# Kernel tuning notes

Measured on AMD Instinct MI355X. Metric: run time of the kernel, lower is better.

## Reference

```python
import jax, jax.numpy as jnp
import numpy as np

MAX_DISP = 48
PATCH = 3
OFFSET = 0
PAD = PATCH // 2
EPS = 1e-3


def _unfold(x, P, pad):
    # x: [B,C,H,W] -> [B,C,K2,H,W], K2 enumerated row-major over the PxP window
    B, C, H, W = x.shape
    xp = jnp.pad(x, ((0, 0), (0, 0), (pad, pad), (pad, pad)))
    return jnp.stack([xp[:, :, i:i + H, j:j + W]
                      for i in range(P) for j in range(P)], axis=2)


def _normalize(x, axes):
    # torch F.normalize: x / clamp(||x||_2, min=eps)
    n = jnp.sqrt(jnp.sum(x * x, axis=axes, keepdims=True))
    return x / jnp.maximum(n, EPS)


def setup_inputs() -> dict:
    key = jax.random.key(0)
    k1, k2, k3 = jax.random.split(key, 3)
    shp = (2, 32, 128, 416)
    return {
        "xl": jax.random.normal(k1, shp, dtype=jnp.float32),
        "xm": jax.random.normal(k2, shp, dtype=jnp.float32),
        "xr": jax.random.normal(k3, shp, dtype=jnp.float32),
    }


def reference(xl, xm, xr):
    B, C, H, W = xl.shape
    K2 = PATCH * PATCH
    scale = (C * K2) ** 0.5

    pl = _normalize(_unfold(xl, PATCH, PAD), (1, 2))  # [B,C,K2,H,W]
    pr = _normalize(_unfold(xr, PATCH, PAD), (1, 2))
    fl = _normalize(xm, (1,))                          # [B,C,H,W]

    # fl is constant over the K2 axis, so sum patches over K2 once for sim_L/sim_R
    Sl = pl.sum(axis=2)  # [B,C,H,W]
    Sr = pr.sum(axis=2)

    cL, cR, cLR = [], [], []
    for d in range(OFFSET, OFFSET + MAX_DISP):
        if d > 0:
            # shifted_l[w] = patches_l[w+d] (zero right pad); shifted_r[w] = patches_r[w-d]
            sL = jnp.einsum('bchw,bchw->bhw', fl[..., :W - d], Sl[..., d:])
            sL = jnp.pad(sL, ((0, 0), (0, 0), (0, d)))
            sR = jnp.einsum('bchw,bchw->bhw', fl[..., d:], Sr[..., :W - d])
            sR = jnp.pad(sR, ((0, 0), (0, 0), (d, 0)))
            wlr = W - 2 * d  # overlap region of the two opposite shifts
            if wlr > 0:
                sLR = jnp.einsum('bckhw,bckhw->bhw', pl[..., 2 * d:], pr[..., :wlr])
                sLR = jnp.pad(sLR, ((0, 0), (0, 0), (d, d)))
            else:
                sLR = jnp.zeros((B, H, W), xl.dtype)
        else:
            sL = jnp.einsum('bchw,bchw->bhw', fl, Sl)
            sR = jnp.einsum('bchw,bchw->bhw', fl, Sr)
            sLR = jnp.einsum('bckhw,bckhw->bhw', pl, pr)
        cL.append(sL / scale)
        cR.append(sR / scale)
        cLR.append(sLR / scale)

    cost = jnp.stack([jnp.stack(cL, 1), jnp.stack(cR, 1), jnp.stack(cLR, 1)], axis=1)
    return jnp.clip(cost, -10.0, 10.0).astype(jnp.float16)  # [B,3,D,H,W]
```

## Files before the change

### kernel.cpp

```cpp
#include <hip/hip_runtime.h>
#include <math.h>

#define B 2
#define C 32
#define H 128
#define W 416
#define D 48
#define HW (H*W)
#define CHW (C*HW)
#define EPSN 1e-3f
#define ISCALE 0.05892556509887896f
#define LSTR 36
#define DSPL (D / 2)

__device__ __forceinline__ float clip10(float x) {
    return fminf(fmaxf(x, -10.0f), 10.0f);
}

__global__ __launch_bounds__(256) void k_sq(const float* __restrict__ xl,
                                            const float* __restrict__ xr,
                                            const float* __restrict__ xm,
                                            float* __restrict__ sql,
                                            float* __restrict__ sqr,
                                            float* __restrict__ inm) {
    int idx = blockIdx.x * 256 + threadIdx.x;
    if (idx >= B * HW) return;
    int b = idx / HW, hw = idx - b * HW;
    const float* pl = xl + (size_t)b * CHW + hw;
    const float* pr = xr + (size_t)b * CHW + hw;
    const float* pm = xm + (size_t)b * CHW + hw;
    float al = 0.f, ar = 0.f, am = 0.f;
#pragma unroll
    for (int c = 0; c < C; ++c) {
        float vl = pl[c * HW], vr = pr[c * HW], vm = pm[c * HW];
        al += vl * vl; ar += vr * vr; am += vm * vm;
    }
    sql[idx] = al;
    sqr[idx] = ar;
    inm[idx] = 1.0f / fmaxf(sqrtf(am), EPSN);
}

__global__ __launch_bounds__(256) void k_norm(const float* __restrict__ sql,
                                              const float* __restrict__ sqr,
                                              float* __restrict__ inl,
                                              float* __restrict__ inr) {
    int idx = blockIdx.x * 256 + threadIdx.x;
    if (idx >= B * HW) return;
    int b = idx / HW, hw = idx - b * HW;
    int h = hw / W, w = hw - h * W;
    float sl = 0.f, sr = 0.f;
#pragma unroll
    for (int di = -1; di <= 1; ++di) {
        int hh = h + di;
        if (hh < 0 || hh >= H) continue;
#pragma unroll
        for (int dj = -1; dj <= 1; ++dj) {
            int ww = w + dj;
            if (ww < 0 || ww >= W) continue;
            int p = b * HW + hh * W + ww;
            sl += sql[p];
            sr += sqr[p];
        }
    }
    inl[idx] = 1.0f / fmaxf(sqrtf(sl), EPSN);
    inr[idx] = 1.0f / fmaxf(sqrtf(sr), EPSN);
}

__global__ __launch_bounds__(256) void k_box(const float* __restrict__ xl,
                                             const float* __restrict__ xr,
                                             float* __restrict__ boxl,
                                             float* __restrict__ boxr) {
    int idx = blockIdx.x * 256 + threadIdx.x;
    int w4 = (idx % (W / 4)) * 4;
    int h = (idx / (W / 4)) % H;
    int rest = idx / (H * (W / 4));
    size_t base = (size_t)rest * HW;
    float4 al = {0.f, 0.f, 0.f, 0.f}, ar = {0.f, 0.f, 0.f, 0.f};
#pragma unroll
    for (int dh = -1; dh <= 1; ++dh) {
        int hh = h + dh;
        if (hh < 0 || hh >= H) continue;
        const float* rl = xl + base + hh * W;
        const float* rr = xr + base + hh * W;
        float4 m = *(const float4*)(rl + w4);
        float lm = (w4 > 0) ? rl[w4 - 1] : 0.f;
        float rm = (w4 + 4 < W) ? rl[w4 + 4] : 0.f;
        al.x += lm + m.x + m.y;  al.y += m.x + m.y + m.z;
        al.z += m.y + m.z + m.w; al.w += m.z + m.w + rm;
        float4 n = *(const float4*)(rr + w4);
        float ln = (w4 > 0) ? rr[w4 - 1] : 0.f;
        float rn = (w4 + 4 < W) ? rr[w4 + 4] : 0.f;
        ar.x += ln + n.x + n.y;  ar.y += n.x + n.y + n.z;
        ar.z += n.y + n.z + n.w; ar.w += n.z + n.w + rn;
    }
    *(float4*)(boxl + base + h * W + w4) = al;
    *(float4*)(boxr + base + h * W + w4) = ar;
}

__device__ __forceinline__ void stage_row_v2(const float* __restrict__ gsrc,
                                             float* __restrict__ lds,
                                             int tid, int nthreads) {
    for (int t = tid; t < (W / 4) * C; t += nthreads) {
        int rw = t & 7;
        int cl = (t >> 3) & 7;
        int g  = t >> 6;
        int wg = g % 13;
        int ch = g / 13;
        int c  = ch * 8 + cl;
        int w4 = (wg * 8 + rw) * 4;
        float4 v = *(const float4*)(gsrc + (size_t)c * HW + w4);
        lds[(w4 + 0) * LSTR + c] = v.x;
        lds[(w4 + 1) * LSTR + c] = v.y;
        lds[(w4 + 2) * LSTR + c] = v.z;
        lds[(w4 + 3) * LSTR + c] = v.w;
    }
}

__device__ __forceinline__ float dot32(const float* __restrict__ fl,
                                       const float* __restrict__ col) {
    const float4* c4 = (const float4*)col;
    float a = 0.0f;
#pragma unroll
    for (int q = 0; q < 8; ++q) {
        float4 v = c4[q];
        a += fl[4 * q + 0] * v.x + fl[4 * q + 1] * v.y
           + fl[4 * q + 2] * v.z + fl[4 * q + 3] * v.w;
    }
    return a;
}

__device__ __forceinline__ void dot32x2(const float* __restrict__ fl0,
                                        const float* __restrict__ fl1,
                                        const float* __restrict__ col,
                                        float& a0, float& a1) {
    const float4* c4 = (const float4*)col;
    float s0 = 0.f, s1 = 0.f;
#pragma unroll
    for (int q = 0; q < 8; ++q) {
        float4 v = c4[q];
        s0 += fl0[4 * q + 0] * v.x + fl0[4 * q + 1] * v.y
            + fl0[4 * q + 2] * v.z + fl0[4 * q + 3] * v.w;
        s1 += fl1[4 * q + 0] * v.x + fl1[4 * q + 1] * v.y
            + fl1[4 * q + 2] * v.z + fl1[4 * q + 3] * v.w;
    }
    a0 = s0; a1 = s1;
}

__global__ __launch_bounds__(256) void k_lr(const float* __restrict__ xm,
                                            const float* __restrict__ boxl,
                                            const float* __restrict__ boxr,
                                            const float* __restrict__ inl,
                                            const float* __restrict__ inr,
                                            const float* __restrict__ inm,
                                            float* __restrict__ out) {
    __shared__ float sB[W * LSTR];
    __shared__ float sIn[W];
    int tid = threadIdx.x;
    int h = blockIdx.x;
    int b = blockIdx.y;
    int d0 = blockIdx.z * DSPL;
    bool act = tid < (W / 2);
    int w = 2 * tid;
    int bhw = b * HW + h * W;
    const float* pm = xm + (size_t)b * CHW + h * W;

    float fl0[C], fl1[C];
    if (act) {
        float2 im = *(const float2*)(inm + bhw + w);
#pragma unroll
        for (int c = 0; c < C; ++c) {
            float2 mv = *(const float2*)(pm + c * HW + w);
            fl0[c] = mv.x * im.x;
            fl1[c] = mv.y * im.y;
        }
    } else {
#pragma unroll
        for (int c = 0; c < C; ++c) { fl0[c] = 0.f; fl1[c] = 0.f; }
    }

    stage_row_v2(boxl + (size_t)b * CHW + h * W, sB, tid, 256);
    for (int j = tid; j < W; j += 256) sIn[j] = inl[bhw + j];
    __syncthreads();
    if (act) {
        float* o = out + ((size_t)b * 3 + 0) * D * HW + h * W;
        float a0p = 0.f;
#pragma unroll 4
        for (int j = 0; j <= DSPL; ++j) {
            int v = w + d0 + j;
            float a0 = 0.f, a1 = 0.f;
            if (v < W) {
                dot32x2(fl0, fl1, sB + v * LSTR, a0, a1);
                float s = sIn[v] * ISCALE;
                a0 = clip10(a0 * s);
                a1 = clip10(a1 * s);
            }
            if (j >= 1) {
                int d = d0 + j - 1;
                *(float2*)(o + (size_t)d * HW + w) = make_float2(a0p, a1);
            }
            a0p = a0;
        }
    }
    __syncthreads();

    stage_row_v2(boxr + (size_t)b * CHW + h * W, sB, tid, 256);
    for (int j = tid; j < W; j += 256) sIn[j] = inr[bhw + j];
    __syncthreads();
    if (act) {
        float* o = out + ((size_t)b * 3 + 1) * D * HW + h * W;
        float a0p = 0.f;
#pragma unroll 4
        for (int j = 0; j <= DSPL; ++j) {
            int v = w - d0 - (DSPL - 1) + j;
            float a0 = 0.f, a1 = 0.f;
            if (v >= 0) {
                dot32x2(fl0, fl1, sB + v * LSTR, a0, a1);
                float s = sIn[v] * ISCALE;
                a0 = clip10(a0 * s);
                a1 = clip10(a1 * s);
            }
            if (j >= 1) {
                int d = d0 + DSPL - j;
                *(float2*)(o + (size_t)d * HW + w) = make_float2(a0p, a1);
            }
            a0p = a0;
        }
    }
}

__global__ __launch_bounds__(448) void k_e(const float* __restrict__ xl,
                                           const float* __restrict__ xr,
                                           float* __restrict__ EH) {
    __shared__ float sXL[W * LSTR];
    int tid = threadIdx.x;
    int h = blockIdx.x;
    int b = blockIdx.y;
    int d0 = blockIdx.z * DSPL;
    int lane = tid & 63;
    int wv = tid >> 6;
    int v = wv * 62 + lane - 1;
    bool vin = (v >= 0) && (v < W);
    const float* br = xr + (size_t)b * CHW + h * W;

    float xrv[C];
#pragma unroll
    for (int c = 0; c < C; ++c) xrv[c] = vin ? br[c * HW + v] : 0.0f;

    stage_row_v2(xl + (size_t)b * CHW + h * W, sXL, tid, 448);
    __syncthreads();

    bool wr = (lane >= 1) && (lane <= 62) && (v < W);
    float* pe = EH + (((size_t)b * D) * H + h) * W + v;
    for (int d = d0; d < d0 + DSPL; ++d) {
        int s = 2 * d;
        float e = 0.0f;
        if (vin && v + s < W) e = dot32(xrv, sXL + (v + s) * LSTR);
        float em = __shfl_up(e, 1);
        float ep = __shfl_down(e, 1);
        float eh = em + e + ep;
        if (wr) pe[(size_t)d * HW] = eh;
    }
}

#define DCH 12
__global__ __launch_bounds__(448) void k_lr2(const float* __restrict__ EH,
                                             const float* __restrict__ inl,
                                             const float* __restrict__ inr,
                                             float* __restrict__ out) {
    int w = threadIdx.x;
    int dc = blockIdx.x;
    int h = blockIdx.y;
    int b = blockIdx.z;
    if (w >= W) return;
    int bhw = b * HW + h * W;
    bool hm = (h > 0), hp = (h < H - 1);

    float* o = out + ((size_t)b * 3 + 2) * D * HW + h * W + w;
#pragma unroll
    for (int i = 0; i < DCH; ++i) {
        int d = dc * DCH + i;
        float r = 0.0f;
        if (w >= d && w + d < W) {
            int vc = w - d;
            const float* base = EH + ((size_t)b * D + d) * HW + vc;
            float e = base[h * W];
            if (hm) e += base[(h - 1) * W];
            if (hp) e += base[(h + 1) * W];
            float nl = inl[bhw + w + d];
            float nr = inr[bhw + vc];
            r = clip10(e * nl * nr * ISCALE);
        }
        o[(size_t)d * HW] = r;
    }
}

extern "C" void kernel_launch(void* const* d_in, const int* in_sizes, int n_in,
                              void* d_out, int out_size, void* d_ws, size_t ws_size,
                              hipStream_t stream) {
    const float* xl = (const float*)d_in[0];
    const float* xm = (const float*)d_in[1];
    const float* xr = (const float*)d_in[2];
    float* out = (float*)d_out;

    float* ws = (float*)d_ws;
    float* boxl = ws;
    float* boxr = boxl + (size_t)B * CHW;
    float* inl  = boxr + (size_t)B * CHW;
    float* inr  = inl + B * HW;
    float* inm  = inr + B * HW;
    float* sql  = inm + B * HW;
    float* sqr  = sql + B * HW;
    float* EH   = sqr + B * HW;

    k_sq<<<dim3((B * HW + 255) / 256), dim3(256), 0, stream>>>(xl, xr, xm, sql, sqr, inm);
    k_norm<<<dim3((B * HW + 255) / 256), dim3(256), 0, stream>>>(sql, sqr, inl, inr);
    k_box<<<dim3((B * CHW / 4 + 255) / 256), dim3(256), 0, stream>>>(xl, xr, boxl, boxr);
    k_e<<<dim3(H, B, 2), dim3(448), 0, stream>>>(xl, xr, EH);
    k_lr<<<dim3(H, B, 2), dim3(256), 0, stream>>>(xm, boxl, boxr, inl, inr, inm, out);
    k_lr2<<<dim3(4, H, B), dim3(448), 0, stream>>>(EH, inl, inr, out);
}
```

Baseline: 191.3 us.

## Fuse box filter, squared norms and xm norm into consumer kernels

Removes the separate k_sq and k_box kernels. Vertical box sums are now computed while staging rows into LDS, and horizontal box sums come from a sliding three-tap window over the per-column dot products. The xm inverse norm is computed inside k_lr, and the squared norms of xl and xr are computed in k_e from data it already loads. This cuts two launches and the round trip of the full box-filtered tensors through global memory, at the cost of extra row loads per staging pass and a few more loop iterations.

Measured after the change: 164.6 us. 14.0% less time.

```diff
diff --git a/kernel.cpp b/kernel.cpp
--- a/kernel.cpp
+++ b/kernel.cpp
@@ -17,29 +17,6 @@
     return fminf(fmaxf(x, -10.0f), 10.0f);
 }
 
-__global__ __launch_bounds__(256) void k_sq(const float* __restrict__ xl,
-                                            const float* __restrict__ xr,
-                                            const float* __restrict__ xm,
-                                            float* __restrict__ sql,
-                                            float* __restrict__ sqr,
-                                            float* __restrict__ inm) {
-    int idx = blockIdx.x * 256 + threadIdx.x;
-    if (idx >= B * HW) return;
-    int b = idx / HW, hw = idx - b * HW;
-    const float* pl = xl + (size_t)b * CHW + hw;
-    const float* pr = xr + (size_t)b * CHW + hw;
-    const float* pm = xm + (size_t)b * CHW + hw;
-    float al = 0.f, ar = 0.f, am = 0.f;
-#pragma unroll
-    for (int c = 0; c < C; ++c) {
-        float vl = pl[c * HW], vr = pr[c * HW], vm = pm[c * HW];
-        al += vl * vl; ar += vr * vr; am += vm * vm;
-    }
-    sql[idx] = al;
-    sqr[idx] = ar;
-    inm[idx] = 1.0f / fmaxf(sqrtf(am), EPSN);
-}
-
 __global__ __launch_bounds__(256) void k_norm(const float* __restrict__ sql,
                                               const float* __restrict__ sqr,
                                               float* __restrict__ inl,
@@ -64,37 +41,6 @@
     }
     inl[idx] = 1.0f / fmaxf(sqrtf(sl), EPSN);
     inr[idx] = 1.0f / fmaxf(sqrtf(sr), EPSN);
-}
-
-__global__ __launch_bounds__(256) void k_box(const float* __restrict__ xl,
-                                             const float* __restrict__ xr,
-                                             float* __restrict__ boxl,
-                                             float* __restrict__ boxr) {
-    int idx = blockIdx.x * 256 + threadIdx.x;
-    int w4 = (idx % (W / 4)) * 4;
-    int h = (idx / (W / 4)) % H;
-    int rest = idx / (H * (W / 4));
-    size_t base = (size_t)rest * HW;
-    float4 al = {0.f, 0.f, 0.f, 0.f}, ar = {0.f, 0.f, 0.f, 0.f};
-#pragma unroll
-    for (int dh = -1; dh <= 1; ++dh) {
-        int hh = h + dh;
-        if (hh < 0 || hh >= H) continue;
-        const float* rl = xl + base + hh * W;
-        const float* rr = xr + base + hh * W;
-        float4 m = *(const float4*)(rl + w4);
-        float lm = (w4 > 0) ? rl[w4 - 1] : 0.f;
-        float rm = (w4 + 4 < W) ? rl[w4 + 4] : 0.f;
-        al.x += lm + m.x + m.y;  al.y += m.x + m.y + m.z;
-        al.z += m.y + m.z + m.w; al.w += m.z + m.w + rm;
-        float4 n = *(const float4*)(rr + w4);
-        float ln = (w4 > 0) ? rr[w4 - 1] : 0.f;
-        float rn = (w4 + 4 < W) ? rr[w4 + 4] : 0.f;
-        ar.x += ln + n.x + n.y;  ar.y += n.x + n.y + n.z;
-        ar.z += n.y + n.z + n.w; ar.w += n.z + n.w + rn;
-    }
-    *(float4*)(boxl + base + h * W + w4) = al;
-    *(float4*)(boxr + base + h * W + w4) = ar;
 }
 
 __device__ __forceinline__ void stage_row_v2(const float* __restrict__ gsrc,
@@ -116,6 +62,34 @@
     }
 }
 
+__device__ __forceinline__ void stage_row3_v2(const float* __restrict__ gsrc,
+                                              float* __restrict__ lds,
+                                              int h, int tid, int nthreads) {
+    for (int t = tid; t < (W / 4) * C; t += nthreads) {
+        int rw = t & 7;
+        int cl = (t >> 3) & 7;
+        int g  = t >> 6;
+        int wg = g % 13;
+        int ch = g / 13;
+        int c  = ch * 8 + cl;
+        int w4 = (wg * 8 + rw) * 4;
+        const float* p = gsrc + (size_t)c * HW + w4;
+        float4 v = *(const float4*)(p);
+        if (h > 0) {
+            float4 a = *(const float4*)(p - W);
+            v.x += a.x; v.y += a.y; v.z += a.z; v.w += a.w;
+        }
+        if (h < H - 1) {
+            float4 a = *(const float4*)(p + W);
+            v.x += a.x; v.y += a.y; v.z += a.z; v.w += a.w;
+        }
+        lds[(w4 + 0) * LSTR + c] = v.x;
+        lds[(w4 + 1) * LSTR + c] = v.y;
+        lds[(w4 + 2) * LSTR + c] = v.z;
+        lds[(w4 + 3) * LSTR + c] = v.w;
+    }
+}
+
 __device__ __forceinline__ float dot32(const float* __restrict__ fl,
                                        const float* __restrict__ col) {
     const float4* c4 = (const float4*)col;
@@ -147,11 +121,10 @@
 }
 
 __global__ __launch_bounds__(256) void k_lr(const float* __restrict__ xm,
-                                            const float* __restrict__ boxl,
-                                            const float* __restrict__ boxr,
+                                            const float* __restrict__ xl,
+                                            const float* __restrict__ xr,
                                             const float* __restrict__ inl,
                                             const float* __restrict__ inr,
-                                            const float* __restrict__ inm,
                                             float* __restrict__ out) {
     __shared__ float sB[W * LSTR];
     __shared__ float sIn[W];
@@ -166,71 +139,89 @@
 
     float fl0[C], fl1[C];
     if (act) {
-        float2 im = *(const float2*)(inm + bhw + w);
+        float am0 = 0.f, am1 = 0.f;
 #pragma unroll
         for (int c = 0; c < C; ++c) {
             float2 mv = *(const float2*)(pm + c * HW + w);
-            fl0[c] = mv.x * im.x;
-            fl1[c] = mv.y * im.y;
-        }
+            fl0[c] = mv.x; fl1[c] = mv.y;
+            am0 += mv.x * mv.x; am1 += mv.y * mv.y;
+        }
+        float im0 = 1.0f / fmaxf(sqrtf(am0), EPSN);
+        float im1 = 1.0f / fmaxf(sqrtf(am1), EPSN);
+#pragma unroll
+        for (int c = 0; c < C; ++c) { fl0[c] *= im0; fl1[c] *= im1; }
     } else {
 #pragma unroll
         for (int c = 0; c < C; ++c) { fl0[c] = 0.f; fl1[c] = 0.f; }
     }
 
-    stage_row_v2(boxl + (size_t)b * CHW + h * W, sB, tid, 256);
+    stage_row3_v2(xl + (size_t)b * CHW + h * W, sB, h, tid, 256);
     for (int j = tid; j < W; j += 256) sIn[j] = inl[bhw + j];
     __syncthreads();
     if (act) {
         float* o = out + ((size_t)b * 3 + 0) * D * HW + h * W;
-        float a0p = 0.f;
+        float g0a = 0.f, g0b = 0.f, g1a = 0.f, g1b = 0.f, s0p = 0.f;
 #pragma unroll 4
-        for (int j = 0; j <= DSPL; ++j) {
-            int v = w + d0 + j;
-            float a0 = 0.f, a1 = 0.f;
-            if (v < W) {
-                dot32x2(fl0, fl1, sB + v * LSTR, a0, a1);
-                float s = sIn[v] * ISCALE;
-                a0 = clip10(a0 * s);
-                a1 = clip10(a1 * s);
+        for (int j = 0; j <= DSPL + 2; ++j) {
+            int v = w + d0 - 1 + j;
+            float c0 = 0.f, c1 = 0.f;
+            if (v >= 0 && v < W) dot32x2(fl0, fl1, sB + v * LSTR, c0, c1);
+            float s0 = 0.f, s1 = 0.f;
+            if (j >= 2) {
+                int m = v - 1;
+                if (m < W) {
+                    float sc = sIn[m] * ISCALE;
+                    s0 = clip10((g0a + g0b + c0) * sc);
+                    s1 = clip10((g1a + g1b + c1) * sc);
+                }
+                if (j >= 3) {
+                    int d = d0 + j - 3;
+                    *(float2*)(o + (size_t)d * HW + w) = make_float2(s0p, s1);
+                }
             }
-            if (j >= 1) {
-                int d = d0 + j - 1;
-                *(float2*)(o + (size_t)d * HW + w) = make_float2(a0p, a1);
-            }
-            a0p = a0;
+            s0p = s0;
+            g0a = g0b; g0b = c0;
+            g1a = g1b; g1b = c1;
         }
     }
     __syncthreads();
 
-    stage_row_v2(boxr + (size_t)b * CHW + h * W, sB, tid, 256);
+    stage_row3_v2(xr + (size_t)b * CHW + h * W, sB, h, tid, 256);
     for (int j = tid; j < W; j += 256) sIn[j] = inr[bhw + j];
     __syncthreads();
     if (act) {
         float* o = out + ((size_t)b * 3 + 1) * D * HW + h * W;
-        float a0p = 0.f;
+        float g0a = 0.f, g0b = 0.f, g1a = 0.f, g1b = 0.f, s0p = 0.f;
 #pragma unroll 4
-        for (int j = 0; j <= DSPL; ++j) {
-            int v = w - d0 - (DSPL - 1) + j;
-            float a0 = 0.f, a1 = 0.f;
-            if (v >= 0) {
-                dot32x2(fl0, fl1, sB + v * LSTR, a0, a1);
-                float s = sIn[v] * ISCALE;
-                a0 = clip10(a0 * s);
-                a1 = clip10(a1 * s);
+        for (int j = 0; j <= DSPL + 2; ++j) {
+            int v = w - d0 - DSPL + j;
+            float c0 = 0.f, c1 = 0.f;
+            if (v >= 0 && v < W) dot32x2(fl0, fl1, sB + v * LSTR, c0, c1);
+            float s0 = 0.f, s1 = 0.f;
+            if (j >= 2) {
+                int m = v - 1;
+                if (m >= 0) {
+                    float sc = sIn[m] * ISCALE;
+                    s0 = clip10((g0a + g0b + c0) * sc);
+                    s1 = clip10((g1a + g1b + c1) * sc);
+                }
+                if (j >= 3) {
+                    int d = d0 + DSPL + 2 - j;
+                    *(float2*)(o + (size_t)d * HW + w) = make_float2(s0p, s1);
+                }
             }
-            if (j >= 1) {
-                int d = d0 + DSPL - j;
-                *(float2*)(o + (size_t)d * HW + w) = make_float2(a0p, a1);
-            }
-            a0p = a0;
+            s0p = s0;
+            g0a = g0b; g0b = c0;
+            g1a = g1b; g1b = c1;
         }
     }
 }
 
 __global__ __launch_bounds__(448) void k_e(const float* __restrict__ xl,
                                            const float* __restrict__ xr,
-                                           float* __restrict__ EH) {
+                                           float* __restrict__ EH,
+                                           float* __restrict__ sql,
+                                           float* __restrict__ sqr) {
     __shared__ float sXL[W * LSTR];
     int tid = threadIdx.x;
     int h = blockIdx.x;
@@ -250,6 +241,25 @@
     __syncthreads();
 
     bool wr = (lane >= 1) && (lane <= 62) && (v < W);
+
+    if (blockIdx.z == 0) {
+        float sr_ = 0.f, sl_ = 0.f;
+#pragma unroll
+        for (int c = 0; c < C; ++c) sr_ += xrv[c] * xrv[c];
+        if (vin) {
+            const float4* c4 = (const float4*)(sXL + v * LSTR);
+#pragma unroll
+            for (int q = 0; q < 8; ++q) {
+                float4 x = c4[q];
+                sl_ += x.x * x.x + x.y * x.y + x.z * x.z + x.w * x.w;
+            }
+        }
+        if (wr) {
+            sqr[b * HW + h * W + v] = sr_;
+            sql[b * HW + h * W + v] = sl_;
+        }
+    }
+
     float* pe = EH + (((size_t)b * D) * H + h) * W + v;
     for (int d = d0; d < d0 + DSPL; ++d) {
         int s = 2 * d;
@@ -303,19 +313,14 @@
     float* out = (float*)d_out;
 
     float* ws = (float*)d_ws;
-    float* boxl = ws;
-    float* boxr = boxl + (size_t)B * CHW;
-    float* inl  = boxr + (size_t)B * CHW;
-    float* inr  = inl + B * HW;
-    float* inm  = inr + B * HW;
-    float* sql  = inm + B * HW;
-    float* sqr  = sql + B * HW;
-    float* EH   = sqr + B * HW;
-
-    k_sq<<<dim3((B * HW + 255) / 256), dim3(256), 0, stream>>>(xl, xr, xm, sql, sqr, inm);
+    float* inl = ws;
+    float* inr = inl + B * HW;
+    float* sql = inr + B * HW;
+    float* sqr = sql + B * HW;
+    float* EH  = sqr + B * HW;
+
+    k_e<<<dim3(H, B, 2), dim3(448), 0, stream>>>(xl, xr, EH, sql, sqr);
     k_norm<<<dim3((B * HW + 255) / 256), dim3(256), 0, stream>>>(sql, sqr, inl, inr);
-    k_box<<<dim3((B * CHW / 4 + 255) / 256), dim3(256), 0, stream>>>(xl, xr, boxl, boxr);
-    k_e<<<dim3(H, B, 2), dim3(448), 0, stream>>>(xl, xr, EH);
-    k_lr<<<dim3(H, B, 2), dim3(256), 0, stream>>>(xm, boxl, boxr, inl, inr, inm, out);
+    k_lr<<<dim3(H, B, 2), dim3(256), 0, stream>>>(xm, xl, xr, inl, inr, out);
     k_lr2<<<dim3(4, H, B), dim3(448), 0, stream>>>(EH, inl, inr, out);
 }
```
